# Optimization experiments

Measured on AMD Instinct MI355X. Metric: run time of the kernel, lower is better.

## Reference

```python
import jax, jax.numpy as jnp
import numpy as np


def setup_inputs() -> dict:
    key = jax.random.key(0)
    B, T, F = 128, 16384, 4
    x = jax.random.normal(key, (B, T, F), dtype=jnp.float32)
    return {"x": x, "wow": 16}


def reference(x, wow):
    # x: (B, T, F). Circular sliding-window unfold:
    # out[b, t] = concat_{k=0..wow-1} x[b, (t - wow + 1 + k) mod T, :]
    # This matches: prepend the last (wow-1) timesteps, then take every
    # length-wow window, stacked along a new axis, flattened with F.
    B, T, F = x.shape
    # idx[t, k] = (t - wow + 1 + k) mod T  -> shape (T, wow)
    idx = (jnp.arange(T)[:, None] + jnp.arange(-wow + 1, 1)[None, :]) % T
    windows = x[:, idx, :]            # (B, T, wow, F) single fused gather
    return windows.reshape(B, T, wow * F)
```

## Files before the change

### kernel.cpp

```cpp
#include <hip/hip_runtime.h>


__global__ __launch_bounds__(256) void ring_pad_kernel(
    const float4* __restrict__ x, float4* __restrict__ out, int total) {
    constexpr int WOW = 16;
    constexpr int T   = 16384;
    constexpr int SHIFT = T - WOW + 1;

    int stride = gridDim.x * blockDim.x;
    for (int i = blockIdx.x * blockDim.x + threadIdx.x; i < total; i += stride) {
        int w = i & (WOW - 1);
        int t = (i >> 4) & (T - 1);
        int b = i >> 18;
        int src = (t + w + SHIFT) & (T - 1);
        out[i] = x[b * T + src];
    }
}

extern "C" void kernel_launch(void* const* d_in, const int* in_sizes, int n_in,
                              void* d_out, int out_size, void* d_ws, size_t ws_size,
                              hipStream_t stream) {
    const float4* x = (const float4*)d_in[0];
    float4* out = (float4*)d_out;

    int total = out_size / 4;
    int threads = 256;
    int blocks = 8192;
    ring_pad_kernel<<<blocks, threads, 0, stream>>>(x, out, total);
}
```

Before: 121.8 us.

## Stage input tile in LDS and emit windows with nontemporal stores

Each block now handles one batch row and a 256-timestep tile. It loads that tile plus a 15-row halo into shared memory once, and every output window is then read from LDS. This replaces the 16x-redundant global gathers, and output writes use nontemporal stores so the 128 MB output does not pollute the cache. The kernel hardcodes the grid shape and drops the grid-stride loop, and it adds a barrier per block.

```diff
diff --git a/kernel.cpp b/kernel.cpp
--- a/kernel.cpp
+++ b/kernel.cpp
@@ -1,30 +1,43 @@
 #include <hip/hip_runtime.h>
 
 
+typedef float f32x4 __attribute__((ext_vector_type(4)));
+
 __global__ __launch_bounds__(256) void ring_pad_kernel(
-    const float4* __restrict__ x, float4* __restrict__ out, int total) {
-    constexpr int WOW = 16;
-    constexpr int T   = 16384;
-    constexpr int SHIFT = T - WOW + 1;
+    const f32x4* __restrict__ x, f32x4* __restrict__ out) {
+    constexpr int T     = 16384;
+    constexpr int WOW   = 16;
+    constexpr int LROWS = 256 + WOW - 1;
 
-    int stride = gridDim.x * blockDim.x;
-    for (int i = blockIdx.x * blockDim.x + threadIdx.x; i < total; i += stride) {
-        int w = i & (WOW - 1);
-        int t = (i >> 4) & (T - 1);
-        int b = i >> 18;
-        int src = (t + w + SHIFT) & (T - 1);
-        out[i] = x[b * T + src];
+    __shared__ f32x4 lx[LROWS];
+
+    int b  = blockIdx.x >> 6;
+    int t0 = (blockIdx.x & 63) << 8;
+    int k  = threadIdx.x;
+
+    const f32x4* xb = x + (size_t)b * T;
+    lx[k] = xb[(t0 - (WOW - 1) + k) & (T - 1)];
+    if (k < LROWS - 256)
+        lx[k + 256] = xb[(t0 - (WOW - 1) + k + 256) & (T - 1)];
+    __syncthreads();
+
+    int w  = k & (WOW - 1);
+    int tl = k >> 4;
+    f32x4* ob = out + ((size_t)(b * T + t0) << 4);
+
+    #pragma unroll
+    for (int it = 0; it < 16; ++it) {
+        f32x4 v = lx[it * 16 + tl + w];
+        __builtin_nontemporal_store(v, &ob[it * 256 + k]);
     }
 }
 
 extern "C" void kernel_launch(void* const* d_in, const int* in_sizes, int n_in,
                               void* d_out, int out_size, void* d_ws, size_t ws_size,
                               hipStream_t stream) {
-    const float4* x = (const float4*)d_in[0];
-    float4* out = (float4*)d_out;
+    const f32x4* x = (const f32x4*)d_in[0];
+    f32x4* out = (f32x4*)d_out;
 
-    int total = out_size / 4;
-    int threads = 256;
-    int blocks = 8192;
-    ring_pad_kernel<<<blocks, threads, 0, stream>>>(x, out, total);
+    int blocks = 128 * 64;
+    ring_pad_kernel<<<blocks, 256, 0, stream>>>(x, out);
 }
```

Result: faster. 112.3 us (-7.8%).
